# Kernel optimization log

Measured on AMD Instinct MI355X. Metric: run time of the kernel, lower is better.

## Reference

```python
import jax, jax.numpy as jnp
import numpy as np
import math

RADIUS = 0.2
NSAMPLE = 32
M = 8
EPS = 1e-6

def _normalize(v, axis):
    n = jnp.sqrt(jnp.sum(v * v, axis=axis, keepdims=True))
    return v / (n + EPS)

def _ball_query(xyz, new_xyz, fps_idx):
    # Emulates pointnet2 ball_query: first NSAMPLE in-radius indices in scan
    # order, padded with the first found index; rows with no hits stay 0.
    B, N, _ = xyz.shape
    d2 = jnp.sum((new_xyz[:, :, None, :] - xyz[:, None, :, :]) ** 2, axis=-1)  # (B,P,N)
    mask = d2 < RADIUS * RADIUS
    keys = jnp.where(mask, jnp.arange(N, dtype=jnp.int32)[None, None, :], N)
    neg_top, _ = jax.lax.top_k(-keys, NSAMPLE)
    sorted_idx = -neg_top  # ascending first NSAMPLE in-radius indices (or N pads)
    cnt = jnp.sum(mask, axis=-1, keepdims=True)
    first = jnp.where(cnt > 0, jnp.minimum(sorted_idx[..., :1], N - 1), 0)
    j = jnp.arange(NSAMPLE)[None, None, :]
    idx = jnp.where(j < cnt, sorted_idx, first).astype(jnp.int32)
    return jnp.concatenate([fps_idx[:, :, None].astype(jnp.int32), idx], axis=-1)  # (B,P,S+1)

def _group(features, idx):
    # features (B,C,N), idx (B,P,S) -> (B,C,P,S)
    return jax.vmap(lambda f, i: f[:, i])(features, idx)

def _project_one(p):
    # reference vector in plane orthogonal to normalized p; p (B,3,P,1)
    p = _normalize(p, 1)
    px, py, pz = p[:, 0], p[:, 1], p[:, 2]
    colin = jnp.abs(px) > 1.0 - 1e-3
    rx = jnp.where(colin, -py * px, 1.0 - px * px)
    ry = jnp.where(colin, 1.0 - py * py, -px * py)
    rz = jnp.where(colin, -py * pz, -px * pz)
    return _normalize(jnp.stack([rx, ry, rz], axis=1), 1)

def _rot_sort(p, pts):
    # sort pts (B,3,P,S) along S by clockwise angle of projection onto plane orthogonal to p
    p = _normalize(p, 1)
    ref = _project_one(p)
    vert = jnp.sum(p * pts, axis=1, keepdims=True) * p
    projs = _normalize(pts - vert, 1)
    refb = jnp.broadcast_to(ref, projs.shape)
    sinus = jnp.sum(jnp.cross(refb, projs, axis=1) * p, axis=1, keepdims=True)
    cosinus = jnp.sum(refb * projs, axis=1, keepdims=True)
    angles = jnp.arctan2(sinus, cosinus)  # (B,1,P,S)
    close = jnp.sum(projs * projs, axis=1, keepdims=True) < 1e-12
    rnd = (jax.random.uniform(jax.random.key(42), angles.shape) - 0.5) * (2.0 * math.pi)
    angles = jnp.where(close, rnd, angles)
    ind = jnp.argsort(angles, axis=-1)
    return jnp.take_along_axis(pts, jnp.broadcast_to(ind, pts.shape), axis=-1)

def _calc_invariance(center, rel):
    norm2 = jnp.sqrt(jnp.sum(rel * rel, axis=1, keepdims=True) + 1e-12)
    c = _normalize(center, 1)
    cosang = jnp.sum(c * rel, axis=1, keepdims=True) / norm2
    angle = jnp.arccos(jnp.clip(cosang, -1.0 + EPS, 1.0 - EPS))
    return jnp.concatenate([norm2, angle], axis=1)  # (B,2,P,S)

def _to_quat(xyz):
    dist = jnp.sqrt(jnp.sum(xyz * xyz, axis=1, keepdims=True))
    ori = xyz / (dist + EPS)
    theta = dist / RADIUS * (math.pi / 2.0)
    return jnp.concatenate([jnp.cos(theta), jnp.sin(theta) * ori], axis=1)  # (B,4,P,S)

def _forward(xyz, new_xyz, fps_idx):
    idx = _ball_query(xyz, new_xyz, fps_idx)                 # (B,P,S+1)
    grouped = _group(jnp.swapaxes(xyz, 1, 2), idx)           # (B,3,P,S+1)
    centers = jnp.swapaxes(new_xyz, 1, 2)[..., None]         # (B,3,P,1)
    grouped = _rot_sort(centers, grouped[..., 1:] - centers) # (B,3,P,S)
    inv = _calc_invariance(centers, grouped)                 # (B,2,P,S)
    q = _to_quat(grouped)                                    # (B,4,P,S)
    quats = jnp.stack([jnp.roll(q, -m, axis=-1) for m in range(M)], axis=2)  # (B,4,M,P,S)
    B, _, _, P, S = quats.shape
    quats = quats.reshape(B, 4 * M, P, S)
    return jnp.concatenate([inv, quats], axis=1)             # (B,34,P,S)

def setup_inputs() -> dict:
    key = jax.random.key(0)
    k1, k2 = jax.random.split(key)
    B, N, P = 4, 8192, 2048
    xyz = jax.random.uniform(k1, (B, N, 3), dtype=jnp.float32)
    fps_idx = jax.random.randint(k2, (B, P), 0, N, dtype=jnp.int32)
    new_xyz = jax.vmap(lambda x, i: x[i])(xyz, fps_idx)
    return {"xyz": xyz, "new_xyz": new_xyz, "fps_idx": fps_idx}

def reference(xyz, new_xyz, fps_idx):
    return _forward(xyz, new_xyz, fps_idx)
```

## Files before the change

kernel.cpp:

```cpp
#include <hip/hip_runtime.h>
#include <math.h>

constexpr int Bc  = 4;
constexpr int Nc  = 8192;
constexpr int Pc  = 2048;
constexpr int Sc  = 32;
constexpr int CHc = 34;
constexpr int WSTRIDE = 40;
constexpr int NQ  = Bc * Pc;
constexpr int SOA_OFF = NQ * WSTRIDE;
constexpr int BN      = Bc * Nc;

#define THREEFRY_PARTITIONABLE 1

#define FMUL __fmul_rn
#define FADD __fadd_rn
#define FSUB __fsub_rn

__device__ __forceinline__ unsigned tf_rotl(unsigned x, int r) {
  return (x << r) | (x >> (32 - r));
}

__device__ __forceinline__ void threefry2x32_k42(unsigned& x0, unsigned& x1) {
  const unsigned ks0 = 0u, ks1 = 42u, ks2 = 0u ^ 42u ^ 0x1BD11BDAu;
  x0 += ks0; x1 += ks1;
#define TF_ROUND(r) { x0 += x1; x1 = tf_rotl(x1, (r)); x1 ^= x0; }
  TF_ROUND(13) TF_ROUND(15) TF_ROUND(26) TF_ROUND(6)
  x0 += ks1; x1 += ks2 + 1u;
  TF_ROUND(17) TF_ROUND(29) TF_ROUND(16) TF_ROUND(24)
  x0 += ks2; x1 += ks0 + 2u;
  TF_ROUND(13) TF_ROUND(15) TF_ROUND(26) TF_ROUND(6)
  x0 += ks0; x1 += ks1 + 3u;
  TF_ROUND(17) TF_ROUND(29) TF_ROUND(16) TF_ROUND(24)
  x0 += ks1; x1 += ks2 + 4u;
  TF_ROUND(13) TF_ROUND(15) TF_ROUND(26) TF_ROUND(6)
  x0 += ks2; x1 += ks0 + 5u;
#undef TF_ROUND
}

__device__ __forceinline__ float jax_rnd_angle(unsigned n) {
#if THREEFRY_PARTITIONABLE
  unsigned x0 = 0u, x1 = n;
  threefry2x32_k42(x0, x1);
  unsigned bits = x0 ^ x1;
#else
  const unsigned half = (unsigned)(Bc * Pc * Sc) / 2u;
  unsigned x0, x1;
  bool second = (n >= half);
  if (second) { x0 = n - half; x1 = n; } else { x0 = n; x1 = n + half; }
  threefry2x32_k42(x0, x1);
  unsigned bits = second ? x1 : x0;
#endif
  float u = __uint_as_float((bits >> 9) | 0x3F800000u) - 1.0f;
  return FMUL(FSUB(u, 0.5f), (float)(2.0 * 3.141592653589793));
}

__device__ __forceinline__ float dot3rn(float ax, float ay, float az,
                                        float bx, float by, float bz) {
  return FADD(FADD(FMUL(ax, bx), FMUL(ay, by)), FMUL(az, bz));
}

__global__ __launch_bounds__(256)
void soa_kernel(const float* __restrict__ xyz, float* __restrict__ wsf)
{
  const int i = blockIdx.x * 256 + threadIdx.x;
  if (i < BN) {
    wsf[SOA_OFF + 0 * BN + i] = xyz[i * 3 + 0];
    wsf[SOA_OFF + 1 * BN + i] = xyz[i * 3 + 1];
    wsf[SOA_OFF + 2 * BN + i] = xyz[i * 3 + 2];
  }
}

__global__ __launch_bounds__(256)
void ball_kernel(const float* __restrict__ wsf,
                 const float* __restrict__ new_xyz,
                 int* __restrict__ ws)
{
  const int wave = threadIdx.x >> 6;
  const int lane = threadIdx.x & 63;
  const int q    = blockIdx.x * 4 + wave;
  const int b    = q >> 11;
  const int p    = q & 2047;

  const float* sxb = wsf + SOA_OFF + 0 * BN + b * Nc;
  const float* syb = wsf + SOA_OFF + 1 * BN + b * Nc;
  const float* szb = wsf + SOA_OFF + 2 * BN + b * Nc;

  const float cx = new_xyz[((size_t)b * Pc + p) * 3 + 0];
  const float cy = new_xyz[((size_t)b * Pc + p) * 3 + 1];
  const float cz = new_xyz[((size_t)b * Pc + p) * 3 + 2];

  int* wq = ws + (size_t)q * WSTRIDE;
  const float R2 = (float)(0.2 * 0.2);
  const unsigned long long below = (1ull << lane) - 1ull;

  int run = 0;
  #pragma unroll 1
  for (int basew = 0; basew < Nc; basew += 512) {
    float xs[8], ys[8], zs[8];
    #pragma unroll
    for (int k = 0; k < 8; ++k) {
      const int i = basew + k * 64 + lane;
      xs[k] = sxb[i];
      ys[k] = syb[i];
      zs[k] = szb[i];
    }
    #pragma unroll
    for (int k = 0; k < 8; ++k) {
      const float dx = FSUB(cx, xs[k]);
      const float dy = FSUB(cy, ys[k]);
      const float dz = FSUB(cz, zs[k]);
      const float d2 = FADD(FADD(FMUL(dx, dx), FMUL(dy, dy)), FMUL(dz, dz));
      const bool m = d2 < R2;
      const unsigned long long mask = __ballot(m);
      if (m) {
        const int pos = run + (int)__popcll(mask & below);
        if (pos < Sc) wq[pos] = basew + k * 64 + lane;
      }
      run += (int)__popcll(mask);
    }
    if (run >= Sc) break;
  }
  if (lane == 0) wq[Sc] = (run > Sc) ? Sc : run;
}

__global__ __launch_bounds__(256)
void emit_kernel(const float* __restrict__ xyz,
                 const float* __restrict__ new_xyz,
                 const int* __restrict__ ws,
                 float* __restrict__ out)
{
  const int wave = threadIdx.x >> 6;
  const int lane = threadIdx.x & 63;
  const int q    = blockIdx.x * 4 + wave;
  const int b    = q >> 11;
  const int p    = q & 2047;

  const float* xb = xyz + (size_t)b * Nc * 3;
  const float cx = new_xyz[((size_t)b * Pc + p) * 3 + 0];
  const float cy = new_xyz[((size_t)b * Pc + p) * 3 + 1];
  const float cz = new_xyz[((size_t)b * Pc + p) * 3 + 2];

  const int* wq = ws + (size_t)q * WSTRIDE;
  const int cnt = wq[Sc];

  const int j  = lane & 31;
  const int gi = wq[(j < cnt) ? j : 0];

  const float ptx = xb[gi * 3 + 0];
  const float pty = xb[gi * 3 + 1];
  const float ptz = xb[gi * 3 + 2];
  const float relx = FSUB(ptx, cx);
  const float rely = FSUB(pty, cy);
  const float relz = FSUB(ptz, cz);

  const float n1  = __fsqrt_rn(dot3rn(cx, cy, cz, cx, cy, cz));
  const float id1 = FADD(n1, 1e-6f);
  const float p1x = __fdiv_rn(cx, id1);
  const float p1y = __fdiv_rn(cy, id1);
  const float p1z = __fdiv_rn(cz, id1);

  const float n2  = __fsqrt_rn(dot3rn(p1x, p1y, p1z, p1x, p1y, p1z));
  const float id2 = FADD(n2, 1e-6f);
  const float p2x = __fdiv_rn(p1x, id2);
  const float p2y = __fdiv_rn(p1y, id2);
  const float p2z = __fdiv_rn(p1z, id2);

  const bool colin = fabsf(p2x) > (float)(1.0 - 0.001);
  const float rxv = colin ? FMUL(-p2y, p2x) : FSUB(1.0f, FMUL(p2x, p2x));
  const float ryv = colin ? FSUB(1.0f, FMUL(p2y, p2y)) : FMUL(-p2x, p2y);
  const float rzv = colin ? FMUL(-p2y, p2z) : FMUL(-p2x, p2z);
  const float nr  = __fsqrt_rn(dot3rn(rxv, ryv, rzv, rxv, ryv, rzv));
  const float idr = FADD(nr, 1e-6f);
  const float refx = __fdiv_rn(rxv, idr);
  const float refy = __fdiv_rn(ryv, idr);
  const float refz = __fdiv_rn(rzv, idr);

  const float sdot = dot3rn(p1x, p1y, p1z, relx, rely, relz);
  const float wx = FSUB(relx, FMUL(sdot, p1x));
  const float wy = FSUB(rely, FMUL(sdot, p1y));
  const float wz = FSUB(relz, FMUL(sdot, p1z));
  const float nw  = __fsqrt_rn(dot3rn(wx, wy, wz, wx, wy, wz));
  const float idw = FADD(nw, 1e-6f);
  const float prx = __fdiv_rn(wx, idw);
  const float pry = __fdiv_rn(wy, idw);
  const float prz = __fdiv_rn(wz, idw);

  const float s2 = dot3rn(prx, pry, prz, prx, pry, prz);

  float angle;
  if (s2 < 1e-12f) {
    const unsigned n = ((unsigned)q << 5) | (unsigned)j;
    angle = jax_rnd_angle(n);
  } else {
    const float ccx = FSUB(FMUL(refy, prz), FMUL(refz, pry));
    const float ccy = FSUB(FMUL(refz, prx), FMUL(refx, prz));
    const float ccz = FSUB(FMUL(refx, pry), FMUL(refy, prx));
    const float sinus   = dot3rn(ccx, ccy, ccz, p1x, p1y, p1z);
    const float cosinus = dot3rn(refx, refy, refz, prx, pry, prz);
    angle = atan2f(sinus, cosinus);
  }

  const unsigned ab   = __float_as_uint(angle);
  const unsigned skey = (ab & 0x80000000u) ? ~ab : (ab | 0x80000000u);
  unsigned long long key = ((unsigned long long)skey << 32) | (unsigned)j;

  #pragma unroll
  for (int k = 2; k <= 32; k <<= 1) {
    #pragma unroll
    for (int jj = k >> 1; jj > 0; jj >>= 1) {
      const unsigned long long other = __shfl_xor(key, jj);
      const bool up      = ((lane & k) == 0);
      const bool lower   = ((lane & jj) == 0);
      const bool takeMin = (lower == up);
      const unsigned long long mn = (key < other) ? key : other;
      const unsigned long long mx = (key < other) ? other : key;
      key = takeMin ? mn : mx;
    }
  }
  const int oj = (int)(key & 31u);

  const float sx = __shfl(relx, oj);
  const float sy = __shfl(rely, oj);
  const float sz = __shfl(relz, oj);

  const float dotr  = sx * sx + sy * sy + sz * sz;
  const float norm2 = sqrtf(dotr + 1e-12f);
  float cosang = (p1x * sx + p1y * sy + p1z * sz) / norm2;
  const float CL = (float)(1.0 - 1e-6);
  cosang = fminf(fmaxf(cosang, -CL), CL);
  const float ainv = acosf(cosang);

  const float dist = sqrtf(dotr);
  const float invd = 1.0f / (dist + 1e-6f);
  const float oxv = sx * invd, oyv = sy * invd, ozv = sz * invd;
  const float theta = (dist / 0.2f) * (float)(3.141592653589793 / 2.0);
  float st, ct;
  sincosf(theta, &st, &ct);
  const float qw = ct, qx = st * oxv, qy = st * oyv, qz = st * ozv;

  const size_t chs   = (size_t)Pc * Sc;
  const size_t baseo = (size_t)b * CHc * chs + (size_t)p * Sc + (size_t)j;

  if (lane < 32) {
    out[baseo + 0 * chs] = norm2;
    out[baseo + 1 * chs] = ainv;
  }
  #pragma unroll
  for (int m = 0; m < 8; ++m) {
    const int src = (j + m) & 31;
    const float vw = __shfl(qw, src);
    const float vx = __shfl(qx, src);
    const float vy = __shfl(qy, src);
    const float vz = __shfl(qz, src);
    if (lane < 32) {
      out[baseo + (size_t)(2 + 0 * 8 + m) * chs] = vw;
      out[baseo + (size_t)(2 + 1 * 8 + m) * chs] = vx;
      out[baseo + (size_t)(2 + 2 * 8 + m) * chs] = vy;
      out[baseo + (size_t)(2 + 3 * 8 + m) * chs] = vz;
    }
  }
}

extern "C" void kernel_launch(void* const* d_in, const int* in_sizes, int n_in,
                              void* d_out, int out_size, void* d_ws, size_t ws_size,
                              hipStream_t stream) {
  const float* xyz     = (const float*)d_in[0];
  const float* new_xyz = (const float*)d_in[1];
  float* out = (float*)d_out;
  int*   ws  = (int*)d_ws;
  float* wsf = (float*)d_ws;

  hipLaunchKernelGGL(soa_kernel, dim3((BN + 255) / 256), dim3(256), 0, stream,
                     xyz, wsf);

  dim3 grid(NQ / 4), block(256);
  hipLaunchKernelGGL(ball_kernel, grid, block, 0, stream, wsf, new_xyz, ws);
  hipLaunchKernelGGL(emit_kernel, grid, block, 0, stream, xyz, new_xyz, ws, out);
}
```

Before: 91.12 us.

## Double-buffer ball-query loads and pack two queries per wave in emit

The ball-query loop now prefetches the next 512-point window into a second register set while the current window is processed, so global load latency overlaps the distance tests and ballots. The emit kernel maps two queries onto each 64-lane wave, one per 32-lane half, with the bitonic sort and shuffles indexed within each half. This halves the emit grid and removes the idle upper half-wave. The cost is more registers in ball_kernel and one possibly wasted prefetch after an early exit.

```diff
diff --git a/kernel.cpp b/kernel.cpp
--- a/kernel.cpp
+++ b/kernel.cpp
@@ -94,10 +94,7 @@
   const float R2 = (float)(0.2 * 0.2);
   const unsigned long long below = (1ull << lane) - 1ull;
 
-  int run = 0;
-  #pragma unroll 1
-  for (int basew = 0; basew < Nc; basew += 512) {
-    float xs[8], ys[8], zs[8];
+  auto loadw = [&](int basew, float xs[8], float ys[8], float zs[8]) {
     #pragma unroll
     for (int k = 0; k < 8; ++k) {
       const int i = basew + k * 64 + lane;
@@ -105,6 +102,9 @@
       ys[k] = syb[i];
       zs[k] = szb[i];
     }
+  };
+  auto procw = [&](int basew, const float xs[8], const float ys[8],
+                   const float zs[8], int& run) {
     #pragma unroll
     for (int k = 0; k < 8; ++k) {
       const float dx = FSUB(cx, xs[k]);
@@ -119,6 +119,18 @@
       }
       run += (int)__popcll(mask);
     }
+  };
+
+  float ax[8], ay[8], az[8], bx[8], by[8], bz[8];
+  loadw(0, ax, ay, az);
+  int run = 0;
+  #pragma unroll 1
+  for (int basew = 0; basew < Nc; basew += 1024) {
+    loadw(basew + 512, bx, by, bz);
+    procw(basew, ax, ay, az, run);
+    if (run >= Sc) break;
+    loadw((basew + 1024) & (Nc - 1), ax, ay, az);
+    procw(basew + 512, bx, by, bz, run);
     if (run >= Sc) break;
   }
   if (lane == 0) wq[Sc] = (run > Sc) ? Sc : run;
@@ -132,7 +144,10 @@
 {
   const int wave = threadIdx.x >> 6;
   const int lane = threadIdx.x & 63;
-  const int q    = blockIdx.x * 4 + wave;
+  const int half = lane >> 5;
+  const int hofs = half << 5;
+  const int j    = lane & 31;
+  const int q    = blockIdx.x * 8 + wave * 2 + half;
   const int b    = q >> 11;
   const int p    = q & 2047;
 
@@ -144,7 +159,6 @@
   const int* wq = ws + (size_t)q * WSTRIDE;
   const int cnt = wq[Sc];
 
-  const int j  = lane & 31;
   const int gi = wq[(j < cnt) ? j : 0];
 
   const float ptx = xb[gi * 3 + 0];
@@ -210,8 +224,8 @@
     #pragma unroll
     for (int jj = k >> 1; jj > 0; jj >>= 1) {
       const unsigned long long other = __shfl_xor(key, jj);
-      const bool up      = ((lane & k) == 0);
-      const bool lower   = ((lane & jj) == 0);
+      const bool up      = ((j & k) == 0);
+      const bool lower   = ((j & jj) == 0);
       const bool takeMin = (lower == up);
       const unsigned long long mn = (key < other) ? key : other;
       const unsigned long long mx = (key < other) ? other : key;
@@ -220,9 +234,9 @@
   }
   const int oj = (int)(key & 31u);
 
-  const float sx = __shfl(relx, oj);
-  const float sy = __shfl(rely, oj);
-  const float sz = __shfl(relz, oj);
+  const float sx = __shfl(relx, oj + hofs);
+  const float sy = __shfl(rely, oj + hofs);
+  const float sz = __shfl(relz, oj + hofs);
 
   const float dotr  = sx * sx + sy * sy + sz * sz;
   const float norm2 = sqrtf(dotr + 1e-12f);
@@ -242,23 +256,19 @@
   const size_t chs   = (size_t)Pc * Sc;
   const size_t baseo = (size_t)b * CHc * chs + (size_t)p * Sc + (size_t)j;
 
-  if (lane < 32) {
-    out[baseo + 0 * chs] = norm2;
-    out[baseo + 1 * chs] = ainv;
-  }
+  out[baseo + 0 * chs] = norm2;
+  out[baseo + 1 * chs] = ainv;
   #pragma unroll
   for (int m = 0; m < 8; ++m) {
-    const int src = (j + m) & 31;
+    const int src = ((j + m) & 31) + hofs;
     const float vw = __shfl(qw, src);
     const float vx = __shfl(qx, src);
     const float vy = __shfl(qy, src);
     const float vz = __shfl(qz, src);
-    if (lane < 32) {
-      out[baseo + (size_t)(2 + 0 * 8 + m) * chs] = vw;
-      out[baseo + (size_t)(2 + 1 * 8 + m) * chs] = vx;
-      out[baseo + (size_t)(2 + 2 * 8 + m) * chs] = vy;
-      out[baseo + (size_t)(2 + 3 * 8 + m) * chs] = vz;
-    }
+    out[baseo + (size_t)(2 + 0 * 8 + m) * chs] = vw;
+    out[baseo + (size_t)(2 + 1 * 8 + m) * chs] = vx;
+    out[baseo + (size_t)(2 + 2 * 8 + m) * chs] = vy;
+    out[baseo + (size_t)(2 + 3 * 8 + m) * chs] = vz;
   }
 }
 
@@ -274,7 +284,9 @@
   hipLaunchKernelGGL(soa_kernel, dim3((BN + 255) / 256), dim3(256), 0, stream,
                      xyz, wsf);
 
-  dim3 grid(NQ / 4), block(256);
-  hipLaunchKernelGGL(ball_kernel, grid, block, 0, stream, wsf, new_xyz, ws);
-  hipLaunchKernelGGL(emit_kernel, grid, block, 0, stream, xyz, new_xyz, ws, out);
-}
+  hipLaunchKernelGGL(ball_kernel, dim3(NQ / 4), dim3(256), 0, stream,
+                     wsf, new_xyz, ws);
+
+  hipLaunchKernelGGL(emit_kernel, dim3(NQ / 8), dim3(256), 0, stream,
+                     xyz, new_xyz, ws, out);
+}
```

Result: faster. 87.04 us (-4.5%).
